# Optimization experiments

Hardware: AMD Instinct MI355X
Metric: run time of the kernel (lower is better)

Reference implementation:

```python
import jax, jax.numpy as jnp
import numpy as np
from jax import lax

NC = 32
EPS = 1e-12


def unfold3x3(x):
    # x: [B,C,H,W] -> [B, C*9, H*W], matching F.unfold(kernel=3, padding=1)
    B, C, H, W = x.shape
    xp = jnp.pad(x, ((0, 0), (0, 0), (1, 1), (1, 1)))
    patches = jnp.stack([xp[:, :, i:i + H, j:j + W]
                         for i in range(3) for j in range(3)], axis=2)  # [B,C,9,H,W]
    return patches.reshape(B, C * 9, H * W)


def fold3x3(u, H, W):
    # u: [B, C*9, H*W] -> [B, C, H, W], matching F.fold(kernel=3, padding=1)
    B = u.shape[0]
    C = u.shape[1] // 9
    p = u.reshape(B, C, 3, 3, H, W)
    out = jnp.zeros((B, C, H + 2, W + 2), u.dtype)
    for i in range(3):
        for j in range(3):
            out = out.at[:, :, i:i + H, j:j + W].add(p[:, :, i, j])
    return out[:, :, 1:H + 1, 1:W + 1]


def l2norm(x, axis):
    n = jnp.sqrt(jnp.sum(x * x, axis=axis, keepdims=True))
    return x / jnp.maximum(n, EPS)


def conv3x3(x, w, b):
    y = lax.conv_general_dilated(x, w, (1, 1), 'SAME',
                                 dimension_numbers=('NCHW', 'OIHW', 'NCHW'))
    return y + b[None, :, None, None]


def setup_inputs() -> dict:
    key = jax.random.key(0)
    k = jax.random.split(key, 6)
    B, C, H, W = 2, NC, 80, 80
    in_HSI = jax.random.normal(k[0], (B, C, H, W), jnp.float32)
    in_PAN = jax.random.normal(k[1], (B, C, H, W), jnp.float32)
    fan1 = 2 * C * 9
    fan2 = C * 9
    w1 = jax.random.normal(k[2], (C, 2 * C, 3, 3), jnp.float32) / np.sqrt(fan1)
    b1 = jax.random.normal(k[3], (C,), jnp.float32) * 0.01
    w2 = jax.random.normal(k[4], (C, C, 3, 3), jnp.float32) / np.sqrt(fan2)
    b2 = jax.random.normal(k[5], (C,), jnp.float32) * 0.01
    return {"in_HSI": in_HSI, "in_PAN": in_PAN, "w1": w1, "b1": b1, "w2": w2, "b2": b2}


def reference(in_HSI, in_PAN, w1, b1, w2, b2):
    B, C, H, W = in_HSI.shape
    L = H * W
    HSI_unfold = unfold3x3(in_HSI)                      # [B, C*9, L]
    PAN_unfold = unfold3x3(in_PAN)                      # [B, C*9, L]
    PAN_q = l2norm(jnp.transpose(PAN_unfold, (0, 2, 1)), axis=2)  # [B, L, C*9]
    HSI_k = l2norm(HSI_unfold, axis=1)                  # [B, C*9, L]
    R = jnp.einsum('blc,bcm->blm', PAN_q, HSI_k)        # [B, L, L]
    R_star = jnp.max(R, axis=1)                         # [B, L]
    R_arg = jnp.argmax(R, axis=1)                       # [B, L]
    # gather columns of unfold(in_PAN) selected by 1-NN indices
    T_unfold = jnp.take_along_axis(PAN_unfold, R_arg[:, None, :], axis=2)
    T_lv3 = fold3x3(T_unfold, H, W) / 9.0               # [B, C, H, W]
    S = R_star.reshape(B, 1, H, W)
    h = jax.nn.relu(conv3x3(jnp.concatenate([T_lv3, in_HSI], axis=1), w1, b1))
    res = conv3x3(h, w2, b2) * S + in_HSI
    return res
```

## Files before the change

### kernel.cpp

```cpp
#include <hip/hip_runtime.h>
#include <hip/hip_bf16.h>
#include <hip/hip_fp16.h>
#include <stdint.h>

#define HH 80
#define WW 80
#define LL 6400
#define CC 32
#define BB 2
#define COG 16
#define DELTA 0.011f
#define NT8 800

typedef __bf16 bf16x8 __attribute__((ext_vector_type(8)));
typedef float  f32x4  __attribute__((ext_vector_type(4)));

__device__ __forceinline__ int div80(int v) {
    return (int)(((unsigned)v * 52429u) >> 22);
}

__device__ __forceinline__ unsigned short f2bf(float f) {
    unsigned int u = __float_as_uint(f);
    return (unsigned short)((u + 0x7fffu + ((u >> 16) & 1u)) >> 16);
}

__device__ __forceinline__ void gload_lds16(void* g, void* l) {
    __builtin_amdgcn_global_load_lds(
        (__attribute__((address_space(1))) void*)g,
        (__attribute__((address_space(3))) void*)l, 16, 0, 0);
}

__global__ __launch_bounds__(256) void fusedunf_kernel(const float* __restrict__ HSI,
                                                       const float* __restrict__ PAN,
                                                       float* __restrict__ invH,
                                                       float* __restrict__ invP,
                                                       float* __restrict__ PANunf,
                                                       float* __restrict__ HSIunf,
                                                       char* __restrict__ Apack,
                                                       char* __restrict__ Bpack) {
    __shared__ float simg[CC][3][82];
    __shared__ float sinv[80];
    const int y = blockIdx.x, mat = blockIdx.y, b = blockIdx.z;
    const int tid = threadIdx.x;
    const float* img = (mat ? HSI : PAN) + (size_t)b * CC * LL;

    for (int i = tid; i < CC * 3; i += 256) {
        simg[i / 3][i % 3][0] = 0.f;
        simg[i / 3][i % 3][81] = 0.f;
    }
    for (int i = tid; i < CC * 3 * 80; i += 256) {
        int c = i / 240, r = i - c * 240;
        int dy = r / 80, x = r - dy * 80;
        int yy = y + dy - 1;
        float v = ((unsigned)yy < 80u) ? img[(size_t)c * LL + yy * 80 + x] : 0.f;
        simg[c][dy][x + 1] = v;
    }
    __syncthreads();

    if (tid < 80) {
        float s = 0.f;
        #pragma unroll 4
        for (int c = 0; c < CC; ++c)
            #pragma unroll
            for (int dy = 0; dy < 3; ++dy)
                #pragma unroll
                for (int dx = 0; dx < 3; ++dx) {
                    float v = simg[c][dy][tid + dx];
                    s = fmaf(v, v, s);
                }
        float inv = 1.f / fmaxf(sqrtf(s), 1e-12f);
        sinv[tid] = inv;
        (mat ? invH : invP)[b * LL + y * 80 + tid] = inv;
    }
    __syncthreads();

    {
        float* unfBase = (mat ? HSIunf : PANunf) + ((size_t)b * LL + y * 80) * 288;
        for (int i = tid; i < 5760; i += 256) {
            const int fidx = i * 4;
            const int l = fidx / 288, k = fidx - l * 288;
            float4 v;
            {
                int kk = k;     int c = kk / 9, t = kk - c * 9; v.x = simg[c][t / 3][l + t % 3];
                kk = k + 1;     c = kk / 9; t = kk - c * 9;     v.y = simg[c][t / 3][l + t % 3];
                kk = k + 2;     c = kk / 9; t = kk - c * 9;     v.z = simg[c][t / 3][l + t % 3];
                kk = k + 3;     c = kk / 9; t = kk - c * 9;     v.w = simg[c][t / 3][l + t % 3];
            }
            *(float4*)(unfBase + fidx) = v;
        }
    }

    {
        char* pk = mat ? Bpack : Apack;
        for (int i = tid; i < 2880; i += 256) {
            const int l = i / 36, g = i - l * 36;
            const float inv = sinv[l];
            unsigned short hs[8];
            #pragma unroll
            for (int jj = 0; jj < 8; ++jj) {
                int kk = g * 8 + jj;
                int c = kk / 9, t = kk - c * 9;
                hs[jj] = f2bf(simg[c][t / 3][l + t % 3] * inv);
            }
            const int q = g / 12;
            const int slot = (g % 12) ^ (l & 15);
            size_t off = ((size_t)(b * 3 + q) * LL + y * 80 + l) * 256 + slot * 16;
            uint4 hv;
            hv.x = hs[0] | ((unsigned)hs[1] << 16); hv.y = hs[2] | ((unsigned)hs[3] << 16);
            hv.z = hs[4] | ((unsigned)hs[5] << 16); hv.w = hs[6] | ((unsigned)hs[7] << 16);
            *(uint4*)(pk + off) = hv;
        }
    }
}

__global__ __launch_bounds__(256, 2) void simq_kernel(const char* __restrict__ Apack,
                                                      const char* __restrict__ Bpack,
                                                      __half* __restrict__ tileMax8) {
    __shared__ __align__(16) char Alds[2][32768];
    const int orig = blockIdx.x;
    const int xcd = orig & 7, idx = orig >> 3;
    const int wg = (xcd < 4 ? xcd * 63 : 252 + (xcd - 4) * 62) + idx;
    const int b = wg / 250;
    int rest = wg - b * 250;
    const int sp = rest / 50;
    const int mt = rest - sp * 50;

    const int tid = threadIdx.x;
    const int lane = tid & 63, w = tid >> 6;
    const int wl = w >> 1, wm = w & 1;
    const int r15 = lane & 15, h = lane >> 4;
    const char* Ab = Apack + (size_t)b * 3 * LL * 256;
    const char* Bb = Bpack + (size_t)b * 3 * LL * 256;
    const int m0 = mt * 128;
    const f32x4 fzero = {0.f, 0.f, 0.f, 0.f};

    bf16x8 bq[3][3][4];
    {
        const int rowb = m0 + wm * 64 + r15;
        #pragma unroll
        for (int c = 0; c < 3; ++c)
            #pragma unroll
            for (int ks = 0; ks < 3; ++ks)
                #pragma unroll
                for (int fm = 0; fm < 4; ++fm) {
                    const int gp = ((ks * 4 + h) ^ r15) * 16;
                    bq[c][ks][fm] = *(const bf16x8*)(Bb + ((size_t)c * LL + rowb + fm * 16) * 256 + gp);
                }
    }

    const char* gAbase = Ab + w * 8192 + lane * 16;
    char* lA0 = Alds[0] + w * 8192;
    char* lA1 = Alds[1] + w * 8192;

    {
        const char* gA = gAbase + ((size_t)(sp * 10) * 128) * 256;
        #pragma unroll
        for (int i = 0; i < 8; ++i) gload_lds16((void*)(gA + i * 1024), lA0 + i * 1024);
    }

    int cur = 0;
    #pragma unroll 1
    for (int lt = 0; lt < 10; ++lt) {
        const int l0 = (sp * 10 + lt) * 128;
        f32x4 acc[4][4];
        #pragma unroll
        for (int i = 0; i < 4; ++i)
            #pragma unroll
            for (int j = 0; j < 4; ++j) acc[i][j] = fzero;

        #pragma unroll
        for (int c = 0; c < 3; ++c) {
            if (c < 2 || lt < 9) {
                const int c2  = (c + 1) % 3;
                const int l0n = (c == 2) ? l0 + 128 : l0;
                const char* gA = gAbase + ((size_t)c2 * LL + l0n) * 256;
                char* lA = (cur ^ 1) ? lA1 : lA0;
                #pragma unroll
                for (int i = 0; i < 8; ++i) gload_lds16((void*)(gA + i * 1024), lA + i * 1024);
                asm volatile("s_waitcnt vmcnt(8)" ::: "memory");
            } else {
                asm volatile("s_waitcnt vmcnt(0)" ::: "memory");
            }
            __builtin_amdgcn_s_barrier();
            asm volatile("" ::: "memory");
            const char* lAr = Alds[cur];
            #pragma unroll
            for (int ks = 0; ks < 3; ++ks) {
                const int gp = ((ks * 4 + h) ^ r15) * 16;
                bf16x8 af[4];
                #pragma unroll
                for (int f = 0; f < 4; ++f)
                    af[f] = *(const bf16x8*)(lAr + (wl * 64 + f * 16 + r15) * 256 + gp);
                #pragma unroll
                for (int fl = 0; fl < 4; ++fl)
                    #pragma unroll
                    for (int fm = 0; fm < 4; ++fm)
                        acc[fl][fm] = __builtin_amdgcn_mfma_f32_16x16x32_bf16(
                            af[fl], bq[c][ks][fm], acc[fl][fm], 0, 0, 0);
            }
            asm volatile("s_waitcnt lgkmcnt(0)" ::: "memory");
            __builtin_amdgcn_s_barrier();
            asm volatile("" ::: "memory");
            cur ^= 1;
        }

        const int Tbase = (sp * 10 + lt) * 16 + wl * 8;
        #pragma unroll
        for (int fl = 0; fl < 4; ++fl) {
            #pragma unroll
            for (int fm = 0; fm < 4; ++fm) {
                f32x4 a = acc[fl][fm];
                float v = fmaxf(fmaxf(a[0], a[1]), fmaxf(a[2], a[3]));
                v = fmaxf(v, __shfl_xor(v, 16, 64));
                if ((h & 1) == 0) {
                    const int m = m0 + wm * 64 + fm * 16 + r15;
                    tileMax8[((size_t)b * LL + m) * NT8 + Tbase + fl * 2 + (h >> 1)] = __float2half(v);
                }
            }
        }
    }
}

__global__ __launch_bounds__(256) void scanfix_kernel(const float* __restrict__ PANunf,
                                                      const float* __restrict__ HSIunf,
                                                      const float* __restrict__ invH,
                                                      const float* __restrict__ invP,
                                                      const __half* __restrict__ tileMax8,
                                                      float* __restrict__ Sv, int* __restrict__ Sa) {
    const int gw = blockIdx.x * 4 + (threadIdx.x >> 6);
    const int lane = threadIdx.x & 63;
    const int b = gw / LL;
    const __half* tm = tileMax8 + (size_t)gw * NT8;

    float tv[13];
    #pragma unroll
    for (int i = 0; i < 13; ++i) {
        int T = i * 64 + lane;
        tv[i] = (T < NT8) ? __half2float(tm[T]) : -3.0e38f;
    }
    float v1 = tv[0];
    #pragma unroll
    for (int i = 1; i < 13; ++i) v1 = fmaxf(v1, tv[i]);
    #pragma unroll
    for (int d = 1; d < 64; d <<= 1) v1 = fmaxf(v1, __shfl_xor(v1, d, 64));
    const float th = v1 - DELTA;

    const float ihm = invH[gw];
    const int lql = lane >> 3, kq = lane & 7;

    float hreg[36];
    {
        const float4* hv4 = (const float4*)(HSIunf + (size_t)gw * 288 + kq * 36);
        #pragma unroll
        for (int j = 0; j < 9; ++j) {
            float4 v = hv4[j];
            hreg[j * 4 + 0] = v.x; hreg[j * 4 + 1] = v.y;
            hreg[j * 4 + 2] = v.z; hreg[j * 4 + 3] = v.w;
        }
    }

    float bv = -3.0e38f; int bl = 0x7fffffff;

    #pragma unroll 1
    for (int i = 0; i < 13; ++i) {
        unsigned long long mask = __ballot(tv[i] >= th);
        while (mask) {
            const int t = __ffsll((long long)mask) - 1;
            mask &= mask - 1;
            const int T = i * 64 + t;
            const int l = T * 8 + lql;
            const float4* pv4 = (const float4*)(PANunf + ((size_t)b * LL + l) * 288 + kq * 36);
            float part = 0.f;
            #pragma unroll
            for (int j = 0; j < 9; ++j) {
                float4 p = pv4[j];
                part = fmaf(p.x, hreg[j * 4 + 0], part);
                part = fmaf(p.y, hreg[j * 4 + 1], part);
                part = fmaf(p.z, hreg[j * 4 + 2], part);
                part = fmaf(p.w, hreg[j * 4 + 3], part);
            }
            part += __shfl_xor(part, 1, 64);
            part += __shfl_xor(part, 2, 64);
            part += __shfl_xor(part, 4, 64);
            const float val = part * invP[b * LL + l] * ihm;
            if (val > bv || (val == bv && l < bl)) { bv = val; bl = l; }
        }
    }
    #pragma unroll
    for (int d = 1; d < 64; d <<= 1) {
        float ov = __shfl_xor(bv, d, 64);
        int   ol = __shfl_xor(bl, d, 64);
        if (ov > bv || (ov == bv && ol < bl)) { bv = ov; bl = ol; }
    }
    if (lane == 0) { Sv[gw] = bv; Sa[gw] = bl; }
}

__global__ void tfold_kernel(const float* __restrict__ PAN, const int* __restrict__ Sa,
                             float* __restrict__ T) {
    int g = blockIdx.x * blockDim.x + threadIdx.x;
    if (g >= BB * CC * LL) return;
    int bc = g / LL, l = g - bc * LL;
    int b = bc >> 5;
    int y = div80(l), x = l - y * 80;
    const float* img = PAN + (size_t)bc * LL;
    const int* Sab = Sa + b * LL;
    float acc = 0.f;
    #pragma unroll
    for (int i = 0; i < 3; ++i) {
        int yp = y + 1 - i;
        if ((unsigned)yp >= 80u) continue;
        #pragma unroll
        for (int j = 0; j < 3; ++j) {
            int xp = x + 1 - j;
            if ((unsigned)xp >= 80u) continue;
            int a = Sab[yp * 80 + xp];
            int ya = div80(a), xa = a - ya * 80;
            int py = ya + i - 1, px = xa + j - 1;
            if ((unsigned)py < 80u && (unsigned)px < 80u) acc += img[py * 80 + px];
        }
    }
    T[g] = acc * (1.f / 9.f);
}

__global__ __launch_bounds__(256) void conv1_kernel(const float* __restrict__ T,
                                                    const float* __restrict__ HSI,
                                                    const float* __restrict__ w1,
                                                    const float* __restrict__ b1,
                                                    float* __restrict__ h) {
    __shared__ __align__(16) float wl[64][9][COG];
    const int tid = threadIdx.x;
    const int co0 = blockIdx.y * COG;
    for (int idx = tid; idx < 64 * 9 * COG; idx += 256) {
        int cog = idx & (COG - 1);
        int rest = idx >> 4;
        int cin = rest / 9, tap = rest - cin * 9;
        wl[cin][tap][cog] = w1[(co0 + cog) * (64 * 9) + cin * 9 + tap];
    }
    __syncthreads();
    const int g = blockIdx.x * 256 + tid;
    const int b = g / LL, l = g - b * LL;
    const int y = div80(l), x = l - y * 80;
    float acc[COG];
    #pragma unroll
    for (int i = 0; i < COG; ++i) acc[i] = 0.f;
    for (int cin = 0; cin < 64; ++cin) {
        const float* img = (cin < CC) ? (T + (size_t)(b * CC + cin) * LL)
                                      : (HSI + (size_t)(b * CC + (cin - CC)) * LL);
        float tap[9];
        #pragma unroll
        for (int i = 0; i < 3; ++i)
            #pragma unroll
            for (int j = 0; j < 3; ++j) {
                int yy = y + i - 1, xx = x + j - 1;
                tap[i * 3 + j] = ((unsigned)yy < 80u && (unsigned)xx < 80u) ? img[yy * 80 + xx] : 0.f;
            }
        #pragma unroll
        for (int t9 = 0; t9 < 9; ++t9) {
            #pragma unroll
            for (int q4 = 0; q4 < COG / 4; ++q4) {
                const float4 wv = *reinterpret_cast<const float4*>(&wl[cin][t9][q4 * 4]);
                acc[q4 * 4 + 0] = fmaf(tap[t9], wv.x, acc[q4 * 4 + 0]);
                acc[q4 * 4 + 1] = fmaf(tap[t9], wv.y, acc[q4 * 4 + 1]);
                acc[q4 * 4 + 2] = fmaf(tap[t9], wv.z, acc[q4 * 4 + 2]);
                acc[q4 * 4 + 3] = fmaf(tap[t9], wv.w, acc[q4 * 4 + 3]);
            }
        }
    }
    #pragma unroll
    for (int cog = 0; cog < COG; ++cog) {
        float v = acc[cog] + b1[co0 + cog];
        h[(size_t)(b * CC + co0 + cog) * LL + l] = fmaxf(v, 0.f);
    }
}

__global__ __launch_bounds__(256) void conv2_kernel(const float* __restrict__ hbuf,
                                                    const float* __restrict__ HSI,
                                                    const float* __restrict__ Sv,
                                                    const float* __restrict__ w2,
                                                    const float* __restrict__ b2,
                                                    float* __restrict__ out) {
    __shared__ __align__(16) float wl[CC][9][COG];
    const int tid = threadIdx.x;
    const int co0 = blockIdx.y * COG;
    for (int idx = tid; idx < CC * 9 * COG; idx += 256) {
        int cog = idx & (COG - 1);
        int rest = idx >> 4;
        int cin = rest / 9, tap = rest - cin * 9;
        wl[cin][tap][cog] = w2[(co0 + cog) * (CC * 9) + cin * 9 + tap];
    }
    __syncthreads();
    const int g = blockIdx.x * 256 + tid;
    const int b = g / LL, l = g - b * LL;
    const int y = div80(l), x = l - y * 80;
    float acc[COG];
    #pragma unroll
    for (int i = 0; i < COG; ++i) acc[i] = 0.f;
    for (int cin = 0; cin < CC; ++cin) {
        const float* img = hbuf + (size_t)(b * CC + cin) * LL;
        float tap[9];
        #pragma unroll
        for (int i = 0; i < 3; ++i)
            #pragma unroll
            for (int j = 0; j < 3; ++j) {
                int yy = y + i - 1, xx = x + j - 1;
                tap[i * 3 + j] = ((unsigned)yy < 80u && (unsigned)xx < 80u) ? img[yy * 80 + xx] : 0.f;
            }
        #pragma unroll
        for (int t9 = 0; t9 < 9; ++t9) {
            #pragma unroll
            for (int q4 = 0; q4 < COG / 4; ++q4) {
                const float4 wv = *reinterpret_cast<const float4*>(&wl[cin][t9][q4 * 4]);
                acc[q4 * 4 + 0] = fmaf(tap[t9], wv.x, acc[q4 * 4 + 0]);
                acc[q4 * 4 + 1] = fmaf(tap[t9], wv.y, acc[q4 * 4 + 1]);
                acc[q4 * 4 + 2] = fmaf(tap[t9], wv.z, acc[q4 * 4 + 2]);
                acc[q4 * 4 + 3] = fmaf(tap[t9], wv.w, acc[q4 * 4 + 3]);
            }
        }
    }
    const float s = Sv[b * LL + l];
    #pragma unroll
    for (int cog = 0; cog < COG; ++cog) {
        int c = co0 + cog;
        out[(size_t)(b * CC + c) * LL + l] = fmaf(acc[cog] + b2[c], s, HSI[(size_t)(b * CC + c) * LL + l]);
    }
}

extern "C" void kernel_launch(void* const* d_in, const int* in_sizes, int n_in,
                              void* d_out, int out_size, void* d_ws, size_t ws_size,
                              hipStream_t stream) {
    const float* HSI = (const float*)d_in[0];
    const float* PAN = (const float*)d_in[1];
    const float* w1  = (const float*)d_in[2];
    const float* b1  = (const float*)d_in[3];
    const float* w2  = (const float*)d_in[4];
    const float* b2  = (const float*)d_in[5];
    float* out = (float*)d_out;

    char* ws = (char*)d_ws;
    size_t off = 0;
    auto alloc = [&](size_t bytes) -> void* {
        void* p = ws + off;
        off += (bytes + 255) & ~(size_t)255;
        return p;
    };
    float* invH  = (float*)alloc((size_t)BB * LL * 4);
    float* invP  = (float*)alloc((size_t)BB * LL * 4);
    char*  Apack = (char*) alloc((size_t)BB * 3 * LL * 256);
    char*  Bpack = (char*) alloc((size_t)BB * 3 * LL * 256);
    __half* tileMax8 = (__half*)alloc((size_t)BB * LL * NT8 * 2);
    float* PANunf = (float*)alloc((size_t)BB * LL * 288 * 4);
    float* HSIunf = (float*)alloc((size_t)BB * LL * 288 * 4);
    float* Sv    = (float*)alloc((size_t)BB * LL * 4);
    int*   Sa    = (int*)  alloc((size_t)BB * LL * 4);
    float* T     = (float*)alloc((size_t)BB * CC * LL * 4);
    float* hbuf  = (float*)alloc((size_t)BB * CC * LL * 4);

    fusedunf_kernel<<<dim3(80, 2, BB), 256, 0, stream>>>(HSI, PAN, invH, invP,
                                                         PANunf, HSIunf, Apack, Bpack);
    simq_kernel<<<dim3(500), 256, 0, stream>>>(Apack, Bpack, tileMax8);
    scanfix_kernel<<<dim3(BB * LL / 4), 256, 0, stream>>>(PANunf, HSIunf, invH, invP, tileMax8, Sv, Sa);
    tfold_kernel<<<dim3((BB * CC * LL + 255) / 256), 256, 0, stream>>>(PAN, Sa, T);
    conv1_kernel<<<dim3(BB * LL / 256, CC / COG), 256, 0, stream>>>(T, HSI, w1, b1, hbuf);
    conv2_kernel<<<dim3(BB * LL / 256, CC / COG), 256, 0, stream>>>(hbuf, HSI, Sv, w2, b2, out);
}
```

Baseline: 221.0 us.

## Stream B fragments from a fragment-packed global layout instead of holding in registers

Before, simq_kernel preloaded all 36 B-operand bf16x8 fragments (144 VGPRs) into registers for the whole block. Now fusedunf writes the HSI-side matrix in a lane-ordered fragment layout, so each 64-lane group reads one contiguous 1 KB chunk. simq then reloads the four B fragments per k-step straight from global/L2 inside the MFMA loop. This frees a large share of registers, which could improve occupancy or scheduling, but adds global-load latency on the critical MFMA path each iteration.

```diff
diff --git a/kernel.cpp b/kernel.cpp
--- a/kernel.cpp
+++ b/kernel.cpp
@@ -11,6 +11,7 @@
 #define COG 16
 #define DELTA 0.011f
 #define NT8 800
+#define PKB ((size_t)400 * 9 * 64 * 16)
 
 typedef __bf16 bf16x8 __attribute__((ext_vector_type(8)));
 typedef float  f32x4  __attribute__((ext_vector_type(4)));
@@ -24,9 +25,9 @@
     return (unsigned short)((u + 0x7fffu + ((u >> 16) & 1u)) >> 16);
 }
 
-__device__ __forceinline__ void gload_lds16(void* g, void* l) {
+__device__ __forceinline__ void gload_lds16(const void* g, void* l) {
     __builtin_amdgcn_global_load_lds(
-        (__attribute__((address_space(1))) void*)g,
+        (const __attribute__((address_space(1))) void*)g,
         (__attribute__((address_space(3))) void*)l, 16, 0, 0);
 }
 
@@ -90,8 +91,8 @@
         }
     }
 
-    {
-        char* pk = mat ? Bpack : Apack;
+    if (mat == 0) {
+        char* pk = Apack;
         for (int i = tid; i < 2880; i += 256) {
             const int l = i / 36, g = i - l * 36;
             const float inv = sinv[l];
@@ -105,6 +106,29 @@
             const int q = g / 12;
             const int slot = (g % 12) ^ (l & 15);
             size_t off = ((size_t)(b * 3 + q) * LL + y * 80 + l) * 256 + slot * 16;
+            uint4 hv;
+            hv.x = hs[0] | ((unsigned)hs[1] << 16); hv.y = hs[2] | ((unsigned)hs[3] << 16);
+            hv.z = hs[4] | ((unsigned)hs[5] << 16); hv.w = hs[6] | ((unsigned)hs[7] << 16);
+            *(uint4*)(pk + off) = hv;
+        }
+    } else {
+        char* pk = Bpack + (size_t)b * PKB;
+        for (int i = tid; i < 2880; i += 256) {
+            const int lane = i & 63;
+            const int rest = i >> 6;
+            const int r16l = rest / 9, kc = rest - r16l * 9;
+            const int r15 = lane & 15, hh = lane >> 4;
+            const int l_loc = r16l * 16 + r15;
+            const float inv = sinv[l_loc];
+            const int k0 = kc * 32 + hh * 8;
+            unsigned short hs[8];
+            #pragma unroll
+            for (int jj = 0; jj < 8; ++jj) {
+                int kk = k0 + jj;
+                int c = kk / 9, t = kk - c * 9;
+                hs[jj] = f2bf(simg[c][t / 3][l_loc + t % 3] * inv);
+            }
+            size_t off = ((((size_t)(y * 5 + r16l)) * 9 + kc) * 64 + lane) * 16;
             uint4 hv;
             hv.x = hs[0] | ((unsigned)hs[1] << 16); hv.y = hs[2] | ((unsigned)hs[3] << 16);
             hv.z = hs[4] | ((unsigned)hs[5] << 16); hv.w = hs[6] | ((unsigned)hs[7] << 16);
@@ -130,23 +154,14 @@
     const int wl = w >> 1, wm = w & 1;
     const int r15 = lane & 15, h = lane >> 4;
     const char* Ab = Apack + (size_t)b * 3 * LL * 256;
-    const char* Bb = Bpack + (size_t)b * 3 * LL * 256;
+    const char* Bb = Bpack + (size_t)b * PKB;
     const int m0 = mt * 128;
+    const int r16b = (m0 >> 4) + wm * 4;
     const f32x4 fzero = {0.f, 0.f, 0.f, 0.f};
 
-    bf16x8 bq[3][3][4];
-    {
-        const int rowb = m0 + wm * 64 + r15;
-        #pragma unroll
-        for (int c = 0; c < 3; ++c)
-            #pragma unroll
-            for (int ks = 0; ks < 3; ++ks)
-                #pragma unroll
-                for (int fm = 0; fm < 4; ++fm) {
-                    const int gp = ((ks * 4 + h) ^ r15) * 16;
-                    bq[c][ks][fm] = *(const bf16x8*)(Bb + ((size_t)c * LL + rowb + fm * 16) * 256 + gp);
-                }
-    }
+    int gp[3];
+    #pragma unroll
+    for (int ks = 0; ks < 3; ++ks) gp[ks] = ((ks * 4 + h) ^ r15) * 16;
 
     const char* gAbase = Ab + w * 8192 + lane * 16;
     char* lA0 = Alds[0] + w * 8192;
@@ -155,7 +170,7 @@
     {
         const char* gA = gAbase + ((size_t)(sp * 10) * 128) * 256;
         #pragma unroll
-        for (int i = 0; i < 8; ++i) gload_lds16((void*)(gA + i * 1024), lA0 + i * 1024);
+        for (int i = 0; i < 8; ++i) gload_lds16(gA + i * 1024, lA0 + i * 1024);
     }
 
     int cur = 0;
@@ -176,7 +191,7 @@
                 const char* gA = gAbase + ((size_t)c2 * LL + l0n) * 256;
                 char* lA = (cur ^ 1) ? lA1 : lA0;
                 #pragma unroll
-                for (int i = 0; i < 8; ++i) gload_lds16((void*)(gA + i * 1024), lA + i * 1024);
+                for (int i = 0; i < 8; ++i) gload_lds16(gA + i * 1024, lA + i * 1024);
                 asm volatile("s_waitcnt vmcnt(8)" ::: "memory");
             } else {
                 asm volatile("s_waitcnt vmcnt(0)" ::: "memory");
@@ -186,17 +201,19 @@
             const char* lAr = Alds[cur];
             #pragma unroll
             for (int ks = 0; ks < 3; ++ks) {
-                const int gp = ((ks * 4 + h) ^ r15) * 16;
-                bf16x8 af[4];
+                const int kc = c * 3 + ks;
+                bf16x8 af[4], bfr[4];
                 #pragma unroll
-                for (int f = 0; f < 4; ++f)
-                    af[f] = *(const bf16x8*)(lAr + (wl * 64 + f * 16 + r15) * 256 + gp);
+                for (int f = 0; f < 4; ++f) {
+                    af[f]  = *(const bf16x8*)(lAr + (wl * 64 + f * 16 + r15) * 256 + gp[ks]);
+                    bfr[f] = *(const bf16x8*)(Bb + ((((size_t)(r16b + f)) * 9 + kc) * 64 + lane) * 16);
+                }
                 #pragma unroll
                 for (int fl = 0; fl < 4; ++fl)
                     #pragma unroll
                     for (int fm = 0; fm < 4; ++fm)
                         acc[fl][fm] = __builtin_amdgcn_mfma_f32_16x16x32_bf16(
-                            af[fl], bq[c][ks][fm], acc[fl][fm], 0, 0, 0);
+                            af[fl], bfr[fm], acc[fl][fm], 0, 0, 0);
             }
             asm volatile("s_waitcnt lgkmcnt(0)" ::: "memory");
             __builtin_amdgcn_s_barrier();
@@ -272,12 +289,12 @@
             const float4* pv4 = (const float4*)(PANunf + ((size_t)b * LL + l) * 288 + kq * 36);
             float part = 0.f;
             #pragma unroll
-            for (int j = 0; j < 9; ++j) {
-                float4 p = pv4[j];
-                part = fmaf(p.x, hreg[j * 4 + 0], part);
-                part = fmaf(p.y, hreg[j * 4 + 1], part);
-                part = fmaf(p.z, hreg[j * 4 + 2], part);
-                part = fmaf(p.w, hreg[j * 4 + 3], part);
+            for (int jj = 0; jj < 9; ++jj) {
+                float4 p = pv4[jj];
+                part = fmaf(p.x, hreg[jj * 4 + 0], part);
+                part = fmaf(p.y, hreg[jj * 4 + 1], part);
+                part = fmaf(p.z, hreg[jj * 4 + 2], part);
+                part = fmaf(p.w, hreg[jj * 4 + 3], part);
             }
             part += __shfl_xor(part, 1, 64);
             part += __shfl_xor(part, 2, 64);
@@ -446,7 +463,7 @@
     float* invH  = (float*)alloc((size_t)BB * LL * 4);
     float* invP  = (float*)alloc((size_t)BB * LL * 4);
     char*  Apack = (char*) alloc((size_t)BB * 3 * LL * 256);
-    char*  Bpack = (char*) alloc((size_t)BB * 3 * LL * 256);
+    char*  Bpack = (char*) alloc((size_t)BB * PKB);
     __half* tileMax8 = (__half*)alloc((size_t)BB * LL * NT8 * 2);
     float* PANunf = (float*)alloc((size_t)BB * LL * 288 * 4);
     float* HSIunf = (float*)alloc((size_t)BB * LL * 288 * 4);
```

New measurement: 237.5 us. 1.07x slower.
